# Optimization experiments

Measured on AMD Instinct MI355X. Metric: run time of the kernel, lower is better.

## Reference

```python
import jax, jax.numpy as jnp
import numpy as np

TAU = 0.01


def setup_inputs() -> dict:
    key = jax.random.key(0)
    k1, k2 = jax.random.split(key)
    N, C = 8192, 256  # N = H*W pixels, C = feature channels
    x_feature = jax.random.normal(k1, (N, C), dtype=jnp.float32)
    y_feature = jax.random.normal(k2, (N, C), dtype=jnp.float32)
    return {"x_feature": x_feature, "y_feature": y_feature}


def reference(x_feature, y_feature):
    # Per-channel L2 normalization (dim=0 in the torch source: norm over pixels)
    x = x_feature / jnp.linalg.norm(x_feature, axis=0, keepdims=True)  # [N, C]
    y = y_feature / jnp.linalg.norm(y_feature, axis=0, keepdims=True)  # [N, C]

    # Dense pixel-pixel cosine correlation matrix
    corr = jnp.einsum('ic,jc->ij', x, y)  # [N, N]

    # Temperature-scaled stable softmax over axis=0 (columns), as in the
    # module's custom softmax (max/sum over dim=0)
    attn = jax.nn.softmax(corr / TAU, axis=0)  # [N, N]

    # Weighted retrieval; only the diagonal of (attn @ y) is kept.
    # diag(attn @ y)[k] = sum_j attn[k, j] * y[j, k] for k < C
    C = y.shape[1]
    warped_color = jnp.einsum('kj,jk->k', attn[:C, :], y[:, :C])  # [C]

    # Confidence map: row-max of the correlation matrix
    confidence_map = jnp.max(corr, axis=1)  # [N]

    return warped_color, confidence_map
```

## Files before the change

### kernel.cpp

```cpp
#include <hip/hip_runtime.h>
#include <hip/hip_bf16.h>

#define NN 8192
#define CC 256
#define ESCALE 144.26950408889634f

typedef __attribute__((ext_vector_type(8))) short short8;
typedef __attribute__((ext_vector_type(4))) float f32x4;

typedef __attribute__((address_space(3))) unsigned int lds_u32;
typedef __attribute__((address_space(1))) const unsigned int glb_u32;

__device__ __forceinline__ void gload16(const ushort* g, ushort* l) {
  __builtin_amdgcn_global_load_lds((glb_u32*)(const void*)g, (lds_u32*)(void*)l, 16, 0, 0);
}

__global__ void colsumsq_kernel(const float* __restrict__ x, const float* __restrict__ y,
                                float* __restrict__ part) {
  const int b = blockIdx.x, t = threadIdx.x;
  const float* src = (b < 256) ? x : y;
  const int bb = b & 255;
  float s = 0.f;
#pragma unroll 4
  for (int r = 0; r < 32; ++r) {
    float v = src[(size_t)(bb * 32 + r) * CC + t];
    s = fmaf(v, v, s);
  }
  part[b * CC + t] = s;
}

__global__ void finnorm_kernel(const float* __restrict__ part, float* __restrict__ inv_n) {
  const int g = blockIdx.x * 4 + (threadIdx.x >> 6);
  const int lane = threadIdx.x & 63;
  const int c = g & 255, T = g >> 8;
  float s = 0.f;
#pragma unroll
  for (int r = 0; r < 4; ++r)
    s += part[(size_t)((T << 8) + lane * 4 + r) * CC + c];
#pragma unroll
  for (int d = 1; d < 64; d <<= 1) s += __shfl_xor(s, d);
  if (lane == 0) inv_n[g] = 1.0f / sqrtf(s);
}

__global__ void normconv_kernel(const float* __restrict__ x, const float* __restrict__ y,
                                const float* __restrict__ inv_n,
                                ushort* __restrict__ xnb, ushort* __restrict__ ynb) {
  int b = blockIdx.x;
  const float* src; ushort* dst; const float* inv;
  if (b < 2048) { src = x; dst = xnb; inv = inv_n; }
  else          { src = y; dst = ynb; inv = inv_n + 256; b -= 2048; }
  const int idx = (b * 256 + threadIdx.x) * 4;
  const float4 v = *(const float4*)(src + idx);
  const int c = idx & (CC - 1);
  __hip_bfloat16 h0 = __float2bfloat16(v.x * inv[c + 0]);
  __hip_bfloat16 h1 = __float2bfloat16(v.y * inv[c + 1]);
  __hip_bfloat16 h2 = __float2bfloat16(v.z * inv[c + 2]);
  __hip_bfloat16 h3 = __float2bfloat16(v.w * inv[c + 3]);
  ushort4 o;
  o.x = *(ushort*)&h0; o.y = *(ushort*)&h1; o.z = *(ushort*)&h2; o.w = *(ushort*)&h3;
  *(ushort4*)(dst + idx) = o;
}

__global__ __launch_bounds__(256, 4)
void gemm_corr_kernel(const ushort* __restrict__ Xn, const ushort* __restrict__ Yn,
                      float* __restrict__ corr_top,
                      float* __restrict__ rowmax_part,
                      float* __restrict__ colsum_part)
{
  const int cb = blockIdx.x, rb = blockIdx.y;
  const int tid = threadIdx.x;
  const int lane = tid & 63, wid = tid >> 6;
  const int wr = wid >> 1, wc = wid & 1;
  const int q = lane >> 4;
  const int lr = lane & 15;

  __shared__ __align__(16) ushort As[128 * 64];
  __shared__ __align__(16) ushort Bs[128 * 64];
  float* redbuf = (float*)As;

  f32x4 acc[4][4];
#pragma unroll
  for (int m = 0; m < 4; ++m)
#pragma unroll
    for (int n = 0; n < 4; ++n) acc[m][n] = (f32x4){0.f, 0.f, 0.f, 0.f};

  const int srow0 = tid >> 3;
  const int sp = (tid & 7) ^ (srow0 & 7);
  const size_t gAb = (size_t)(rb * 128 + srow0) * CC + sp * 8;
  const size_t gBb = (size_t)(cb * 128 + srow0) * CC + sp * 8;

  auto stage = [&](int kt) {
    const int ko = kt * 64;
#pragma unroll
    for (int r = 0; r < 4; ++r) {
      gload16(Xn + gAb + r * 32 * CC + ko, &As[r * 2048 + wid * 512]);
      gload16(Yn + gBb + r * 32 * CC + ko, &Bs[r * 2048 + wid * 512]);
    }
  };

  for (int kt = 0; kt < 4; ++kt) {
    stage(kt);
    __syncthreads();
#pragma unroll
    for (int s = 0; s < 2; ++s) {
      const int sA = ((s * 4 + q) ^ (lr & 7)) * 8;
      short8 af[4], bf[4];
#pragma unroll
      for (int m = 0; m < 4; ++m)
        af[m] = *(const short8*)(&As[(wr * 64 + m * 16 + lr) * 64 + sA]);
#pragma unroll
      for (int n = 0; n < 4; ++n)
        bf[n] = *(const short8*)(&Bs[(wc * 64 + n * 16 + lr) * 64 + sA]);
#pragma unroll
      for (int m = 0; m < 4; ++m)
#pragma unroll
        for (int n = 0; n < 4; ++n)
          acc[m][n] = __builtin_amdgcn_mfma_f32_16x16x32_bf16(af[m], bf[n], acc[m][n], 0, 0, 0);
    }
    __syncthreads();
  }

  if (rb < 2) {
    const int colg = cb * 128 + wc * 64 + lr;
#pragma unroll
    for (int m = 0; m < 4; ++m) {
      const int rowg = rb * 128 + wr * 64 + m * 16 + q * 4;
#pragma unroll
      for (int n = 0; n < 4; ++n)
#pragma unroll
        for (int r = 0; r < 4; ++r)
          corr_top[(size_t)(rowg + r) * NN + colg + n * 16] = acc[m][n][r];
    }
  }

#pragma unroll
  for (int m = 0; m < 4; ++m)
#pragma unroll
    for (int r = 0; r < 4; ++r) {
      float t = fmaxf(fmaxf(acc[m][0][r], acc[m][1][r]), fmaxf(acc[m][2][r], acc[m][3][r]));
      t = fmaxf(t, __shfl_xor(t, 1));
      t = fmaxf(t, __shfl_xor(t, 2));
      t = fmaxf(t, __shfl_xor(t, 4));
      t = fmaxf(t, __shfl_xor(t, 8));
      if (lr == 0) redbuf[wc * 128 + wr * 64 + m * 16 + q * 4 + r] = t;
    }
  __syncthreads();
  if (tid < 128)
    rowmax_part[(size_t)cb * NN + rb * 128 + tid] = fmaxf(redbuf[tid], redbuf[128 + tid]);
  __syncthreads();

#pragma unroll
  for (int n = 0; n < 4; ++n) {
    float s = 0.f;
#pragma unroll
    for (int m = 0; m < 4; ++m)
#pragma unroll
      for (int r = 0; r < 4; ++r)
        s += __builtin_amdgcn_exp2f(acc[m][n][r] * ESCALE);
    s += __shfl_xor(s, 16);
    s += __shfl_xor(s, 32);
    if (lane < 16) redbuf[wr * 128 + wc * 64 + n * 16 + lr] = s;
  }
  __syncthreads();
  if (tid < 128)
    colsum_part[(size_t)rb * NN + cb * 128 + tid] = redbuf[tid] + redbuf[128 + tid];
}

__global__ void reduce_both_kernel(const float* __restrict__ rowmax_part,
                                   const float* __restrict__ colsum_part,
                                   float* __restrict__ out, float* __restrict__ inv_s) {
  const int g = blockIdx.x * 256 + threadIdx.x;
  if (g < 8192) {
    float m = -3.4e38f;
#pragma unroll
    for (int b = 0; b < 64; ++b) m = fmaxf(m, rowmax_part[(size_t)b * NN + g]);
    out[256 + g] = m;
  } else {
    const int j = g - 8192;
    float s = 0.f;
#pragma unroll
    for (int b = 0; b < 64; ++b) s += colsum_part[(size_t)b * NN + j];
    inv_s[j] = 1.0f / s;
  }
}

__global__ void warped_kernel(const float* __restrict__ corr_top, const float* __restrict__ inv_s,
                              const ushort* __restrict__ ynb, float* __restrict__ wpart) {
  const int b = blockIdx.x;
  const int kb = b & 31, jb = b >> 5;
  const int k0 = kb * 8;
  const int t = threadIdx.x;
  const int kk = t & 7, js = t >> 3;
  const int jbase = jb * 2048 + js;
  float p = 0.f;
#pragma unroll 4
  for (int i = 0; i < 64; ++i) {
    const int j = jbase + 32 * i;
    float c = corr_top[(size_t)(k0 + kk) * NN + j];
    float yv = __uint_as_float((unsigned)ynb[(size_t)j * CC + k0 + kk] << 16);
    p += __builtin_amdgcn_exp2f(c * ESCALE) * inv_s[j] * yv;
  }
  p += __shfl_xor(p, 8);
  p += __shfl_xor(p, 16);
  p += __shfl_xor(p, 32);
  __shared__ float lw[4][8];
  const int lane = t & 63, wid = t >> 6;
  if (lane < 8) lw[wid][lane] = p;
  __syncthreads();
  if (t < 8) wpart[jb * 256 + k0 + t] = lw[0][t] + lw[1][t] + lw[2][t] + lw[3][t];
}

__global__ void warpedfin_kernel(const float* __restrict__ wpart, float* __restrict__ out) {
  const int k = threadIdx.x;
  out[k] = wpart[k] + wpart[256 + k] + wpart[512 + k] + wpart[768 + k];
}

extern "C" void kernel_launch(void* const* d_in, const int* in_sizes, int n_in,
                              void* d_out, int out_size, void* d_ws, size_t ws_size,
                              hipStream_t stream) {
  const float* x = (const float*)d_in[0];
  const float* y = (const float*)d_in[1];
  float* out = (float*)d_out;
  char* ws = (char*)d_ws;

  ushort* xnb        = (ushort*)(ws);
  ushort* ynb        = (ushort*)(ws + (4u << 20));
  float*  corr_top   = (float*)(ws + (8u << 20));
  float*  rowmax_prt = (float*)(ws + (16u << 20));
  float*  colsum_prt = (float*)(ws + (18u << 20));
  float*  part       = (float*)(ws + (20u << 20));
  float*  inv_n      = (float*)(ws + (20u << 20) + 524288);
  float*  inv_s      = (float*)(ws + (20u << 20) + 524288 + 4096);

  colsumsq_kernel<<<512, 256, 0, stream>>>(x, y, part);
  finnorm_kernel<<<128, 256, 0, stream>>>(part, inv_n);
  normconv_kernel<<<4096, 256, 0, stream>>>(x, y, inv_n, xnb, ynb);
  gemm_corr_kernel<<<dim3(64, 64), 256, 0, stream>>>(xnb, ynb, corr_top, rowmax_prt, colsum_prt);
  reduce_both_kernel<<<64, 256, 0, stream>>>(rowmax_prt, colsum_prt, out, inv_s);
  warped_kernel<<<128, 256, 0, stream>>>(corr_top, inv_s, ynb, part);
  warpedfin_kernel<<<1, 256, 0, stream>>>(part, out);
}
```

Baseline: 79.34 us.

## Double-buffer GEMM K-tiles with 32-wide stages to overlap loads with MFMA

```diff
diff --git a/kernel.cpp b/kernel.cpp
--- a/kernel.cpp
+++ b/kernel.cpp
@@ -74,8 +74,8 @@
   const int q = lane >> 4;
   const int lr = lane & 15;
 
-  __shared__ __align__(16) ushort As[128 * 64];
-  __shared__ __align__(16) ushort Bs[128 * 64];
+  __shared__ __align__(16) ushort As[2][128 * 32];
+  __shared__ __align__(16) ushort Bs[2][128 * 32];
   float* redbuf = (float*)As;
 
   f32x4 acc[4][4];
@@ -84,40 +84,41 @@
 #pragma unroll
     for (int n = 0; n < 4; ++n) acc[m][n] = (f32x4){0.f, 0.f, 0.f, 0.f};
 
-  const int srow0 = tid >> 3;
-  const int sp = (tid & 7) ^ (srow0 & 7);
+  const int srow0 = tid >> 2;
+  const int sp = (tid & 3) ^ ((tid >> 3) & 3);
   const size_t gAb = (size_t)(rb * 128 + srow0) * CC + sp * 8;
   const size_t gBb = (size_t)(cb * 128 + srow0) * CC + sp * 8;
 
-  auto stage = [&](int kt) {
-    const int ko = kt * 64;
-#pragma unroll
-    for (int r = 0; r < 4; ++r) {
-      gload16(Xn + gAb + r * 32 * CC + ko, &As[r * 2048 + wid * 512]);
-      gload16(Yn + gBb + r * 32 * CC + ko, &Bs[r * 2048 + wid * 512]);
-    }
+  auto stage = [&](int b, int kt) {
+    const int ko = kt * 32;
+    gload16(Xn + gAb + ko,               &As[b][wid * 512]);
+    gload16(Xn + gAb + 64 * CC + ko,     &As[b][2048 + wid * 512]);
+    gload16(Yn + gBb + ko,               &Bs[b][wid * 512]);
+    gload16(Yn + gBb + 64 * CC + ko,     &Bs[b][2048 + wid * 512]);
   };
 
-  for (int kt = 0; kt < 4; ++kt) {
-    stage(kt);
+  stage(0, 0);
+  __syncthreads();
+
+  int cur = 0;
+#pragma unroll
+  for (int kk = 0; kk < 8; ++kk) {
+    if (kk < 7) stage(cur ^ 1, kk + 1);
+    const int sA = (q ^ ((lr >> 1) & 3)) * 8;
+    short8 af[4], bf[4];
+#pragma unroll
+    for (int m = 0; m < 4; ++m)
+      af[m] = *(const short8*)(&As[cur][(wr * 64 + m * 16 + lr) * 32 + sA]);
+#pragma unroll
+    for (int n = 0; n < 4; ++n)
+      bf[n] = *(const short8*)(&Bs[cur][(wc * 64 + n * 16 + lr) * 32 + sA]);
+#pragma unroll
+    for (int m = 0; m < 4; ++m)
+#pragma unroll
+      for (int n = 0; n < 4; ++n)
+        acc[m][n] = __builtin_amdgcn_mfma_f32_16x16x32_bf16(af[m], bf[n], acc[m][n], 0, 0, 0);
     __syncthreads();
-#pragma unroll
-    for (int s = 0; s < 2; ++s) {
-      const int sA = ((s * 4 + q) ^ (lr & 7)) * 8;
-      short8 af[4], bf[4];
-#pragma unroll
-      for (int m = 0; m < 4; ++m)
-        af[m] = *(const short8*)(&As[(wr * 64 + m * 16 + lr) * 64 + sA]);
-#pragma unroll
-      for (int n = 0; n < 4; ++n)
-        bf[n] = *(const short8*)(&Bs[(wc * 64 + n * 16 + lr) * 64 + sA]);
-#pragma unroll
-      for (int m = 0; m < 4; ++m)
-#pragma unroll
-        for (int n = 0; n < 4; ++n)
-          acc[m][n] = __builtin_amdgcn_mfma_f32_16x16x32_bf16(af[m], bf[n], acc[m][n], 0, 0, 0);
-    }
-    __syncthreads();
+    cur ^= 1;
   }
 
   if (rb < 2) {
```

After: 82.87 us. 1.04x slower.
